# Kernel tuning notes

Hardware: AMD Instinct MI355X
Metric: run time of the kernel (lower is better)

## Reference

```python
import jax, jax.numpy as jnp
import numpy as np

IN_DIM = 256
OUT_DIM = 256
B, N = 8, 2048


def setup_inputs() -> dict:
    key = jax.random.key(0)
    k1, k2, k3 = jax.random.split(key, 3)
    inp = jax.random.normal(k1, (B, N, IN_DIM), dtype=jnp.float32)
    # binary adjacency mask, stored as float (it is multiplied into the scores)
    adj = jax.random.randint(k2, (B, N, N), 0, 2).astype(jnp.float32)
    # orthogonal init for W (as in nn.init.orthogonal_), zeros for b
    g = np.random.default_rng(0).normal(size=(IN_DIM, OUT_DIM)).astype(np.float32)
    q, r = np.linalg.qr(g)
    q = q * np.sign(np.diag(r))  # make init deterministic-signed like torch
    W = jnp.asarray(q, dtype=jnp.float32)
    b = jnp.zeros((OUT_DIM,), dtype=jnp.float32)
    return {"inp": inp, "adj": adj, "W": W, "b": b}


def reference(inp, adj, W, b):
    feat_dim = inp.shape[-1]
    # [B,N,N] raw scores, scaled by sqrt(d); NOTE: no max-subtraction, faithful to source
    scores = jnp.einsum("bnd,bmd->bnm", inp, inp) / jnp.sqrt(jnp.float32(feat_dim))
    exp_scores = jnp.exp(scores) * adj
    denom = jnp.sum(exp_scores, axis=-1, keepdims=True) + 1e-10
    attn = exp_scores / denom                      # [B,N,N]
    out = jnp.einsum("bnm,bmo->bno", attn, inp @ W) + b  # [B,N,OUT_DIM]
    return jax.nn.leaky_relu(out, negative_slope=0.01)
```

## Files before the change

### kernel.cpp

```cpp
#include <hip/hip_runtime.h>
#include <stdint.h>

typedef float    f32x16 __attribute__((ext_vector_type(16)));
typedef uint32_t u32x4  __attribute__((ext_vector_type(4)));
typedef uint32_t u32x2  __attribute__((ext_vector_type(2)));
typedef _Float16 half4  __attribute__((ext_vector_type(4)));

#define DEVI static __device__ __forceinline__
#define NB 8
#define NN 2048
#define ND 256

DEVI void gl_lds16(const void* g, void* l) {
  __builtin_amdgcn_global_load_lds(
      (const __attribute__((address_space(1))) void*)g,
      (__attribute__((address_space(3))) void*)l,
      16, 0, 0);
}

__global__ __launch_bounds__(256) void k_prep(
    const float* __restrict__ adj, const float* __restrict__ inp,
    const float* __restrict__ W,
    _Float16* __restrict__ xh, _Float16* __restrict__ wth,
    _Float16* __restrict__ wtl, uint32_t* __restrict__ bits)
{
  const int blk = blockIdx.x;
  const int tid = threadIdx.x;
  if (blk < 6144) {
    const long long total = 33554432LL;
    const long long stride = 6144LL * 256;
    const int lane = tid & 63;
    for (long long g = (long long)blk*256 + tid; g < total; g += stride) {
      float v = adj[g];
      unsigned long long m = __ballot(v != 0.0f);
      if (lane == 0)       bits[g >> 5] = (uint32_t)m;
      else if (lane == 32) bits[g >> 5] = (uint32_t)(m >> 32);
    }
  } else if (blk < 6400) {
    int t = (blk - 6144)*256 + tid;
    for (int i = t; i < 1048576; i += 65536) {
      float4 v = ((const float4*)inp)[i];
      half4 h = { (_Float16)v.x, (_Float16)v.y, (_Float16)v.z, (_Float16)v.w };
      *(half4*)(xh + (long long)i*4) = h;
    }
  } else {
    int t = (blk - 6400)*256 + tid;
    for (int i = t; i < 65536; i += 16384) {
      int o = i >> 8, k = i & 255;
      float w = W[k*256 + o];
      _Float16 h = (_Float16)w;
      _Float16 l = (_Float16)(w - (float)h);
      wth[i] = h;
      wtl[i] = l;
    }
  }
}

__global__ __launch_bounds__(256) void k_hgemm(
    const float* __restrict__ x,
    const _Float16* __restrict__ wth, const _Float16* __restrict__ wtl,
    uint16_t* __restrict__ HTh, uint16_t* __restrict__ HTl)
{
  __shared__ __align__(16) _Float16 xs[2][64*256];
  __shared__ __align__(16) uint16_t bnc[2][4][32*36];

  const int tid = threadIdx.x;
  const int lane = tid & 63;
  const int wv = tid >> 6;
  const int ln31 = lane & 31;
  const int hi = lane >> 5;
  const long long rowg0 = (long long)blockIdx.x * 64;

  #pragma unroll
  for (int it = 0; it < 16; ++it) {
    int flat = it*256 + tid;
    int r = flat >> 6;
    int c4 = flat & 63;
    float4 v = ((const float4*)x)[rowg0*64 + flat];
    half4 h = { (_Float16)v.x, (_Float16)v.y, (_Float16)v.z, (_Float16)v.w };
    half4 l = { (_Float16)(v.x - (float)h.x), (_Float16)(v.y - (float)h.y),
                (_Float16)(v.z - (float)h.z), (_Float16)(v.w - (float)h.w) };
    int gr = (c4 >> 1) ^ (r & 7);
    int ad = r*256 + gr*8 + (c4 & 1)*4;
    *(half4*)(xs[0] + ad) = h;
    *(half4*)(xs[1] + ad) = l;
  }
  __syncthreads();

  const int rg = wv >> 1;
  const int og = wv & 1;
  f32x16 acc[4] = {};
  const int arow = rg*32 + ln31;
  #pragma unroll 2
  for (int ks = 0; ks < 16; ++ks) {
    int slot = (ks*2 + hi) ^ (ln31 & 7);
    u32x4 ah = *(const u32x4*)(xs[0] + arow*256 + slot*8);
    u32x4 al = *(const u32x4*)(xs[1] + arow*256 + slot*8);
    #pragma unroll
    for (int ot = 0; ot < 4; ++ot) {
      int o = og*128 + ot*32 + ln31;
      u32x4 bh = *(const u32x4*)(wth + o*256 + ks*16 + hi*8);
      u32x4 bl = *(const u32x4*)(wtl + o*256 + ks*16 + hi*8);
      asm("v_mfma_f32_32x32x16_f16 %0, %1, %2, %0" : "+v"(acc[ot]) : "v"(ah), "v"(bh));
      asm("v_mfma_f32_32x32x16_f16 %0, %1, %2, %0" : "+v"(acc[ot]) : "v"(al), "v"(bh));
      asm("v_mfma_f32_32x32x16_f16 %0, %1, %2, %0" : "+v"(acc[ot]) : "v"(ah), "v"(bl));
    }
  }
  asm volatile("s_nop 7\n\ts_nop 7\n\ts_nop 7");
  __builtin_amdgcn_sched_barrier(0);

  const int bq  = (int)(rowg0 >> 11);
  const int nl0 = (int)(rowg0 & 2047) + rg*32;
  #pragma unroll 1
  for (int ot = 0; ot < 4; ++ot) {
    uint16_t* bh = bnc[0][wv];
    uint16_t* bl = bnc[1][wv];
    #pragma unroll
    for (int r = 0; r < 16; ++r) {
      float v = acc[ot][r];
      uint32_t t = __float_as_uint(v) + 0x8000u;
      float hf = __uint_as_float(t & 0xFFFF0000u);
      uint32_t t2 = __float_as_uint(v - hf) + 0x8000u;
      int n = (r & 3) + 8*(r >> 2) + 4*hi;
      bh[ln31*36 + n] = (uint16_t)(t  >> 16);
      bl[ln31*36 + n] = (uint16_t)(t2 >> 16);
    }
    int orow = lane >> 1, ch = lane & 1;
    const uint16_t* sh = bnc[0][wv] + orow*36 + ch*16;
    const uint16_t* sl = bnc[1][wv] + orow*36 + ch*16;
    u32x2 a0 = *(const u32x2*)(sh + 0);
    u32x2 a1 = *(const u32x2*)(sh + 8);
    u32x2 a2 = *(const u32x2*)(sh + 4);
    u32x2 a3 = *(const u32x2*)(sh + 12);
    u32x4 w0 = { a0.x, a0.y, a1.x, a1.y };
    u32x4 w1 = { a2.x, a2.y, a3.x, a3.y };
    long long off = ((long long)bq*256 + og*128 + ot*32 + orow)*2048 + nl0 + ch*16;
    *(u32x4*)(HTh + off)     = w0;
    *(u32x4*)(HTh + off + 8) = w1;
    u32x2 c0 = *(const u32x2*)(sl + 0);
    u32x2 c1 = *(const u32x2*)(sl + 8);
    u32x2 c2 = *(const u32x2*)(sl + 4);
    u32x2 c3 = *(const u32x2*)(sl + 12);
    u32x4 y0 = { c0.x, c0.y, c1.x, c1.y };
    u32x4 y1 = { c2.x, c2.y, c3.x, c3.y };
    *(u32x4*)(HTl + off)     = y0;
    *(u32x4*)(HTl + off + 8) = y1;
  }
}

template<int MS>
__global__ __launch_bounds__(256, 2) void k_attn(
    const _Float16* __restrict__ xh,
    const uint16_t* __restrict__ HTh, const uint16_t* __restrict__ HTl,
    const uint32_t* __restrict__ bits,
    float* __restrict__ wden, float* __restrict__ wacc,
    const float* __restrict__ bias, float* __restrict__ out)
{
  __shared__ __align__(16) char Ks[16384];
  __shared__ __align__(16) char Hh[20480];
  __shared__ __align__(16) char Hl[20480];
  __shared__ float dls[4][32];

  const int tid  = threadIdx.x;
  const int lane = tid & 63;
  const int wv   = tid >> 6;
  const int hi   = lane >> 5;
  const int ln31 = lane & 31;

  int ms, b, n0idx;
  if (MS == 4) {
    int xcd = blockIdx.x & 7, i = blockIdx.x >> 3;
    int c = xcd*4 + (i & 3);  ms = c >> 3;  b = c & 7;  n0idx = i >> 2;
  } else if (MS == 2) {
    int xcd = blockIdx.x & 7, i = blockIdx.x >> 3;
    int c = xcd*2 + (i & 1);  ms = c >> 3;  b = c & 7;  n0idx = i >> 1;
  } else {
    ms = 0;  b = blockIdx.x & 7;  n0idx = blockIdx.x >> 3;
  }
  const int n0 = n0idx << 7;
  const int nw = n0 + wv*32;
  const int m_begin = ms * (NN / MS);
  const int npass   = (NN / MS) / 32;

  const char* qrow = (const char*)xh + ((long long)(b*NN + nw + ln31)) * 512;
  u32x4 q[16];
  #pragma unroll
  for (int ks = 0; ks < 16; ++ks)
    q[ks] = *(const u32x4*)(qrow + ks*32 + hi*16);

  int koff[4], hoff[5];
  #pragma unroll
  for (int i = 0; i < 4; ++i) {
    int p = wv*4096 + i*1024 + lane*16;
    int r = p >> 9;
    int gs = (p >> 4) & 31;
    koff[i] = r*512 + ((gs ^ (r & 7)) << 4);
  }
  #pragma unroll
  for (int i = 0; i < 5; ++i) {
    int p = wv*5120 + i*1024 + lane*16;
    int r = p / 80;
    int qq = (p - r*80) >> 4;
    qq = (qq == 4) ? 0 : qq;
    hoff[i] = r*4096 + qq*16;
  }
  const char* xb = (const char*)xh  + (long long)b * (NN*512);
  const char* hb = (const char*)HTh + (long long)b * (256*4096);
  const char* lb = (const char*)HTl + (long long)b * (256*4096);
  const uint32_t* brow = bits + (long long)(b*NN + nw + ln31) * 64;

  f32x16 acc[8] = {};
  float den = 0.0f;
  uint32_t bd_cur = brow[m_begin >> 5];

  #pragma unroll 1
  for (int ps = 0; ps < npass; ++ps) {
    const int m0 = m_begin + ps*32;
    const int nwidx = (ps + 1 < npass) ? ((m0 + 32) >> 5) : (m0 >> 5);
    uint32_t bd_nxt = brow[nwidx];
    {
      const char* ksrc = xb + (long long)m0*512;
      #pragma unroll
      for (int i = 0; i < 4; ++i)
        gl_lds16(ksrc + koff[i], Ks + wv*4096 + i*1024);
      const char* hsrc = hb + m0*2;
      const char* lsrc = lb + m0*2;
      #pragma unroll
      for (int i = 0; i < 5; ++i) {
        gl_lds16(hsrc + hoff[i], Hh + wv*5120 + i*1024);
        gl_lds16(lsrc + hoff[i], Hl + wv*5120 + i*1024);
      }
    }
    __syncthreads();

    f32x16 s = {};
    __builtin_amdgcn_s_setprio(1);
    #pragma unroll
    for (int ks = 0; ks < 16; ++ks) {
      int slot = (ks*2 + hi) ^ (ln31 & 7);
      u32x4 a = *(const u32x4*)(Ks + ln31*512 + slot*16);
      asm("v_mfma_f32_32x32x16_f16 %0, %1, %2, %0" : "+v"(s) : "v"(a), "v"(q[ks]));
    }
    __builtin_amdgcn_s_setprio(0);
    asm volatile("s_nop 7\n\ts_nop 7\n\ts_nop 7");
    __builtin_amdgcn_sched_barrier(0);

    const uint32_t bd2 = bd_cur >> (hi*4);
    #pragma unroll
    for (int s2 = 0; s2 < 2; ++s2) {
      uint32_t ph[4], pl[4];
      #pragma unroll
      for (int rp = 0; rp < 4; ++rp) {
        uint32_t hw[2], lw[2];
        #pragma unroll
        for (int e = 0; e < 2; ++e) {
          const int r = s2*8 + rp*2 + e;
          float sv = s[r] * 0.09016844005556021f;
          float ex = __builtin_amdgcn_exp2f(sv);
          const int sh = (r & 3) + ((r >> 2) << 3);
          ex = ((bd2 >> sh) & 1u) ? ex : 0.0f;
          den += ex;
          uint32_t t = __float_as_uint(ex) + 0x8000u;
          hw[e] = t >> 16;
          float hf = __uint_as_float(t & 0xFFFF0000u);
          uint32_t t2 = __float_as_uint(ex - hf) + 0x8000u;
          lw[e] = t2 >> 16;
        }
        ph[rp] = hw[0] | (hw[1] << 16);
        pl[rp] = lw[0] | (lw[1] << 16);
      }
      u32x4 pah = { ph[0], ph[1], ph[2], ph[3] };
      u32x4 pal = { pl[0], pl[1], pl[2], pl[3] };
      __builtin_amdgcn_s_setprio(1);
      #pragma unroll
      for (int ot = 0; ot < 8; ++ot) {
        const int ha = (ot*32 + ln31)*80 + s2*32 + hi*16;
        u32x4 vh = *(const u32x4*)(Hh + ha);
        u32x4 vl = *(const u32x4*)(Hl + ha);
        asm("v_mfma_f32_32x32x16_bf16 %0, %1, %2, %0" : "+v"(acc[ot]) : "v"(pah), "v"(vh));
        asm("v_mfma_f32_32x32x16_bf16 %0, %1, %2, %0" : "+v"(acc[ot]) : "v"(pal), "v"(vh));
        asm("v_mfma_f32_32x32x16_bf16 %0, %1, %2, %0" : "+v"(acc[ot]) : "v"(pah), "v"(vl));
      }
      __builtin_amdgcn_s_setprio(0);
    }
    bd_cur = bd_nxt;
    __syncthreads();
  }

  asm volatile("s_nop 7\n\ts_nop 7\n\ts_nop 7");
  __builtin_amdgcn_sched_barrier(0);
  den += __shfl_xor(den, 32);

  if (MS > 1) {
    float* wa = wacc + (((long long)ms*8 + b)*NN + nw)*256;
    #pragma unroll
    for (int ot = 0; ot < 8; ++ot) {
      #pragma unroll
      for (int r = 0; r < 16; ++r) {
        const int n = (r & 3) + 8*(r >> 2) + 4*hi;
        wa[n*256 + ot*32 + ln31] = acc[ot][r];
      }
    }
    if (lane < 32)
      wden[((long long)ms*8 + b)*NN + nw + ln31] = den;
  } else {
    if (lane < 32) dls[wv][ln31] = den;
    __syncthreads();
    #pragma unroll
    for (int ot = 0; ot < 8; ++ot) {
      const float bi = bias[ot*32 + ln31];
      #pragma unroll
      for (int r = 0; r < 16; ++r) {
        const int n = (r & 3) + 8*(r >> 2) + 4*hi;
        const float dn = dls[wv][n] + 1e-10f;
        float v = acc[ot][r] / dn + bi;
        out[((long long)(b*NN + nw + n))*256 + ot*32 + ln31] = (v > 0.0f) ? v : 0.01f*v;
      }
    }
  }
}

template<int MS>
__global__ __launch_bounds__(256) void k_combine(
    const float* __restrict__ wacc, const float* __restrict__ wden,
    const float* __restrict__ bias, float* __restrict__ out)
{
  const int PLANE = 1048576;
  for (int t = blockIdx.x*256 + threadIdx.x; t < PLANE; t += 2048*256) {
    int row = t >> 6;
    int o4  = t & 63;
    float4 a = ((const float4*)wacc)[t];
    float d = wden[row];
    #pragma unroll
    for (int m = 1; m < MS; ++m) {
      float4 p = ((const float4*)wacc)[t + m*PLANE];
      a.x += p.x; a.y += p.y; a.z += p.z; a.w += p.w;
      d += wden[row + m*16384];
    }
    d += 1e-10f;
    float id = 1.0f / d;
    float4 bi = ((const float4*)bias)[o4];
    float4 r;
    float vx = a.x*id + bi.x; r.x = vx > 0.0f ? vx : 0.01f*vx;
    float vy = a.y*id + bi.y; r.y = vy > 0.0f ? vy : 0.01f*vy;
    float vz = a.z*id + bi.z; r.z = vz > 0.0f ? vz : 0.01f*vz;
    float vw = a.w*id + bi.w; r.w = vw > 0.0f ? vw : 0.01f*vw;
    ((float4*)out)[t] = r;
  }
}

extern "C" void kernel_launch(void* const* d_in, const int* in_sizes, int n_in,
                              void* d_out, int out_size, void* d_ws, size_t ws_size,
                              hipStream_t stream)
{
  const float* inp = (const float*)d_in[0];
  const float* adj = (const float*)d_in[1];
  const float* W   = (const float*)d_in[2];
  const float* bia = (const float*)d_in[3];
  float* out = (float*)d_out;
  char* ws = (char*)d_ws;

  _Float16* xh  = (_Float16*)(ws);
  uint16_t* HTh = (uint16_t*)(ws + 8388608);
  uint16_t* HTl = (uint16_t*)(ws + 16777216);
  _Float16* wth = (_Float16*)(ws + 25165824);
  _Float16* wtl = (_Float16*)(ws + 25296896);
  uint32_t* bt  = (uint32_t*)(ws + 25427968);
  float* den    = (float*)(ws + 29622272);
  float* acc    = (float*)(ws + 29884416);
  const size_t NEED4 = 96993280;
  const size_t NEED2 = 63438848;

  k_prep<<<dim3(6464), dim3(256), 0, stream>>>(adj, inp, W, xh, wth, wtl, bt);
  k_hgemm<<<dim3(256), dim3(256), 0, stream>>>(inp, wth, wtl, HTh, HTl);
  if (ws_size >= NEED4) {
    k_attn<4><<<dim3(512), dim3(256), 0, stream>>>(xh, HTh, HTl, bt, den, acc, nullptr, nullptr);
    k_combine<4><<<dim3(2048), dim3(256), 0, stream>>>(acc, den, bia, out);
  } else if (ws_size >= NEED2) {
    k_attn<2><<<dim3(256), dim3(256), 0, stream>>>(xh, HTh, HTl, bt, den, acc, nullptr, nullptr);
    k_combine<2><<<dim3(2048), dim3(256), 0, stream>>>(acc, den, bia, out);
  } else {
    k_attn<1><<<dim3(128), dim3(256), 0, stream>>>(xh, HTh, HTl, bt, nullptr, nullptr, bia, out);
  }
}
```

Before: 379.6 us.

## Double-buffer K/H tiles with 512-thread blocks sharing each stage

The attention kernel moves to 512-thread blocks covering 256 query rows, so each K/H tile is loaded once per block and shared by eight waves instead of four. The stage buffers are double-buffered in LDS and the next tile's global-to-LDS load is issued before computing the current one, so loads overlap with MFMA work. The score MFMA chain is split into two independent accumulators to shorten the dependency chain. In exchange, occupancy drops to one block per CU, each block uses about 112KB of LDS, and the grid shrinks to 256 blocks.

```diff
diff --git a/kernel.cpp b/kernel.cpp
--- a/kernel.cpp
+++ b/kernel.cpp
@@ -149,17 +149,15 @@
 }
 
 template<int MS>
-__global__ __launch_bounds__(256, 2) void k_attn(
+__global__ __launch_bounds__(512, 1) void k_attn(
     const _Float16* __restrict__ xh,
     const uint16_t* __restrict__ HTh, const uint16_t* __restrict__ HTl,
     const uint32_t* __restrict__ bits,
     float* __restrict__ wden, float* __restrict__ wacc,
     const float* __restrict__ bias, float* __restrict__ out)
 {
-  __shared__ __align__(16) char Ks[16384];
-  __shared__ __align__(16) char Hh[20480];
-  __shared__ __align__(16) char Hl[20480];
-  __shared__ float dls[4][32];
+  __shared__ __align__(16) char L[2][57344];
+  __shared__ float dls[8][32];
 
   const int tid  = threadIdx.x;
   const int lane = tid & 63;
@@ -177,7 +175,7 @@
   } else {
     ms = 0;  b = blockIdx.x & 7;  n0idx = blockIdx.x >> 3;
   }
-  const int n0 = n0idx << 7;
+  const int n0 = n0idx << 8;
   const int nw = n0 + wv*32;
   const int m_begin = ms * (NN / MS);
   const int npass   = (NN / MS) / 32;
@@ -188,21 +186,22 @@
   for (int ks = 0; ks < 16; ++ks)
     q[ks] = *(const u32x4*)(qrow + ks*32 + hi*16);
 
-  int koff[4], hoff[5];
+  int soff[7]; int sel[7];
   #pragma unroll
-  for (int i = 0; i < 4; ++i) {
-    int p = wv*4096 + i*1024 + lane*16;
-    int r = p >> 9;
-    int gs = (p >> 4) & 31;
-    koff[i] = r*512 + ((gs ^ (r & 7)) << 4);
-  }
-  #pragma unroll
-  for (int i = 0; i < 5; ++i) {
-    int p = wv*5120 + i*1024 + lane*16;
-    int r = p / 80;
-    int qq = (p - r*80) >> 4;
-    qq = (qq == 4) ? 0 : qq;
-    hoff[i] = r*4096 + qq*16;
+  for (int j = 0; j < 7; ++j) {
+    int g = wv*7 + j;
+    if (g < 16) {
+      int p = g*1024 + lane*16;
+      int r = p >> 9, gs = (p >> 4) & 31;
+      sel[j] = 0; soff[j] = r*512 + ((gs ^ (r & 7)) << 4);
+    } else {
+      int h = (g < 36) ? (g - 16) : (g - 36);
+      int p = h*1024 + lane*16;
+      int r = p / 80;
+      int qq = (p - r*80) >> 4;
+      qq = (qq == 4) ? 0 : qq;
+      sel[j] = (g < 36) ? 1 : 2; soff[j] = r*4096 + qq*16;
+    }
   }
   const char* xb = (const char*)xh  + (long long)b * (NN*512);
   const char* hb = (const char*)HTh + (long long)b * (256*4096);
@@ -211,39 +210,50 @@
 
   f32x16 acc[8] = {};
   float den = 0.0f;
+
+  #define STAGE(bb, m0v) do {                                          \
+    const char* s0_ = xb + (long long)(m0v)*512;                       \
+    const char* s1_ = hb + (long long)(m0v)*2;                         \
+    const char* s2_ = lb + (long long)(m0v)*2;                         \
+    char* dst_ = L[bb] + (wv*7)*1024;                                  \
+    _Pragma("unroll")                                                  \
+    for (int j = 0; j < 7; ++j) {                                      \
+      const char* sp_ = (sel[j] == 0) ? s0_ : (sel[j] == 1) ? s1_ : s2_; \
+      gl_lds16(sp_ + soff[j], dst_ + j*1024);                          \
+    }                                                                  \
+  } while (0)
+
+  int cur = 0;
+  STAGE(0, m_begin);
   uint32_t bd_cur = brow[m_begin >> 5];
+  __syncthreads();
 
   #pragma unroll 1
   for (int ps = 0; ps < npass; ++ps) {
     const int m0 = m_begin + ps*32;
+    if (ps + 1 < npass) STAGE(cur ^ 1, m0 + 32);
     const int nwidx = (ps + 1 < npass) ? ((m0 + 32) >> 5) : (m0 >> 5);
     uint32_t bd_nxt = brow[nwidx];
-    {
-      const char* ksrc = xb + (long long)m0*512;
-      #pragma unroll
-      for (int i = 0; i < 4; ++i)
-        gl_lds16(ksrc + koff[i], Ks + wv*4096 + i*1024);
-      const char* hsrc = hb + m0*2;
-      const char* lsrc = lb + m0*2;
-      #pragma unroll
-      for (int i = 0; i < 5; ++i) {
-        gl_lds16(hsrc + hoff[i], Hh + wv*5120 + i*1024);
-        gl_lds16(lsrc + hoff[i], Hl + wv*5120 + i*1024);
-      }
-    }
-    __syncthreads();
-
-    f32x16 s = {};
+
+    const char* Kb  = L[cur];
+    const char* HhB = L[cur] + 16384;
+    const char* HlB = L[cur] + 36864;
+
+    f32x16 s0 = {}, s1 = {};
     __builtin_amdgcn_s_setprio(1);
     #pragma unroll
-    for (int ks = 0; ks < 16; ++ks) {
-      int slot = (ks*2 + hi) ^ (ln31 & 7);
-      u32x4 a = *(const u32x4*)(Ks + ln31*512 + slot*16);
-      asm("v_mfma_f32_32x32x16_f16 %0, %1, %2, %0" : "+v"(s) : "v"(a), "v"(q[ks]));
+    for (int ks = 0; ks < 16; ks += 2) {
+      int slot0 = (ks*2 + hi) ^ (ln31 & 7);
+      int slot1 = ((ks+1)*2 + hi) ^ (ln31 & 7);
+      u32x4 a0 = *(const u32x4*)(Kb + ln31*512 + slot0*16);
+      u32x4 a1 = *(const u32x4*)(Kb + ln31*512 + slot1*16);
+      asm("v_mfma_f32_32x32x16_f16 %0, %1, %2, %0" : "+v"(s0) : "v"(a0), "v"(q[ks]));
+      asm("v_mfma_f32_32x32x16_f16 %0, %1, %2, %0" : "+v"(s1) : "v"(a1), "v"(q[ks+1]));
     }
     __builtin_amdgcn_s_setprio(0);
     asm volatile("s_nop 7\n\ts_nop 7\n\ts_nop 7");
     __builtin_amdgcn_sched_barrier(0);
+    f32x16 s = s0 + s1;
 
     const uint32_t bd2 = bd_cur >> (hi*4);
     #pragma unroll
@@ -275,8 +285,8 @@
       #pragma unroll
       for (int ot = 0; ot < 8; ++ot) {
         const int ha = (ot*32 + ln31)*80 + s2*32 + hi*16;
-        u32x4 vh = *(const u32x4*)(Hh + ha);
-        u32x4 vl = *(const u32x4*)(Hl + ha);
+        u32x4 vh = *(const u32x4*)(HhB + ha);
+        u32x4 vl = *(const u32x4*)(HlB + ha);
         asm("v_mfma_f32_32x32x16_bf16 %0, %1, %2, %0" : "+v"(acc[ot]) : "v"(pah), "v"(vh));
         asm("v_mfma_f32_32x32x16_bf16 %0, %1, %2, %0" : "+v"(acc[ot]) : "v"(pal), "v"(vh));
         asm("v_mfma_f32_32x32x16_bf16 %0, %1, %2, %0" : "+v"(acc[ot]) : "v"(pah), "v"(vl));
@@ -285,7 +295,9 @@
     }
     bd_cur = bd_nxt;
     __syncthreads();
-  }
+    cur ^= 1;
+  }
+  #undef STAGE
 
   asm volatile("s_nop 7\n\ts_nop 7\n\ts_nop 7");
   __builtin_amdgcn_sched_barrier(0);
@@ -374,12 +386,12 @@
   k_prep<<<dim3(6464), dim3(256), 0, stream>>>(adj, inp, W, xh, wth, wtl, bt);
   k_hgemm<<<dim3(256), dim3(256), 0, stream>>>(inp, wth, wtl, HTh, HTl);
   if (ws_size >= NEED4) {
-    k_attn<4><<<dim3(512), dim3(256), 0, stream>>>(xh, HTh, HTl, bt, den, acc, nullptr, nullptr);
+    k_attn<4><<<dim3(256), dim3(512), 0, stream>>>(xh, HTh, HTl, bt, den, acc, nullptr, nullptr);
     k_combine<4><<<dim3(2048), dim3(256), 0, stream>>>(acc, den, bia, out);
   } else if (ws_size >= NEED2) {
-    k_attn<2><<<dim3(256), dim3(256), 0, stream>>>(xh, HTh, HTl, bt, den, acc, nullptr, nullptr);
+    k_attn<2><<<dim3(128), dim3(512), 0, stream>>>(xh, HTh, HTl, bt, den, acc, nullptr, nullptr);
     k_combine<2><<<dim3(2048), dim3(256), 0, stream>>>(acc, den, bia, out);
   } else {
-    k_attn<1><<<dim3(128), dim3(256), 0, stream>>>(xh, HTh, HTl, bt, nullptr, nullptr, bia, out);
-  }
-}
+    k_attn<1><<<dim3(64), dim3(512), 0, stream>>>(xh, HTh, HTl, bt, nullptr, nullptr, bia, out);
+  }
+}
```

New measurement: 394.0 us. +3.8%, slower.
